# Kernel optimization log

Measured on AMD Instinct MI355X. Metric: run time of the kernel, lower is better.

The kernel has to match this reference:

```python
import jax, jax.numpy as jnp
import numpy as np

B, S, MD, H = 8, 1024, 1024, 16
D = MD // H  # 64
# Faithful to torch: scale = (dim_per_head // num_heads) ** -0.5 (a quirk, not 1/sqrt(D))
SCALE = float((D // H) ** (-0.5))


def setup_inputs() -> dict:
    k0 = jax.random.key(0)
    ks = jax.random.split(k0, 11)
    w = 1.0 / np.sqrt(MD)
    mk = lambda k, shape, s: jax.random.normal(k, shape, dtype=jnp.float32) * s
    return {
        "query": mk(ks[0], (B, S, MD), 1.0),
        "key": mk(ks[1], (B, S, MD), 1.0),
        "value": mk(ks[2], (B, S, MD), 1.0),
        "Wq": mk(ks[3], (MD, MD), w), "bq": mk(ks[4], (MD,), w),
        "Wk": mk(ks[5], (MD, MD), w), "bk": mk(ks[6], (MD,), w),
        "Wv": mk(ks[7], (MD, MD), w), "bv": mk(ks[8], (MD,), w),
        "Wo": mk(ks[9], (MD, MD), w), "bo": mk(ks[10], (MD,), w),
    }


def reference(query, key, value, Wq, bq, Wk, bk, Wv, bv, Wo, bo):
    # Dropout is identity in eval mode (deterministic reference).
    Bq, T, _ = query.shape
    Sk = key.shape[1]
    q = query @ Wq + bq   # [B, T, H*D]
    k = key @ Wk + bk     # [B, S, H*D]
    v = value @ Wv + bv
    # Faithful replication of torch .view(B*H, -1, D): plain row-major reshape
    # (NOT a head transpose -- it chunks sequence/head indices together).
    q = q.reshape(Bq * H, T, D)
    k = k.reshape(Bq * H, Sk, D)
    v = v.reshape(Bq * H, Sk, D)
    attn = jnp.einsum('btd,bsd->bts', q, k) * SCALE          # [B*H, T, S]
    p = jax.nn.softmax(attn, axis=-1)
    ctx = jnp.einsum('bts,bsd->btd', p, v).reshape(Bq, T, H * D)
    output = ctx @ Wo + bo                                    # [B, T, MD]
    a = attn.reshape(Bq, H, T, Sk)
    attn_post = jax.nn.sigmoid(a).sum(axis=1) / H             # [B, T, S]
    return output, attn_post
```

## Files before the change

kernel.cpp:

```cpp
#include <hip/hip_runtime.h>


typedef __attribute__((ext_vector_type(8))) short bf16x8;
typedef __attribute__((ext_vector_type(4))) float f32x4;
typedef __attribute__((ext_vector_type(4))) int int4v;

static __device__ __forceinline__ short f2bf(float f) {
  union { float f; unsigned u; } v; v.f = f;
  unsigned lsb = (v.u >> 16) & 1u;
  v.u += 0x7fffu + lsb;
  return (short)(v.u >> 16);
}

#define GLDS16(gp, lp) __builtin_amdgcn_global_load_lds( \
    (const __attribute__((address_space(1))) void*)(gp), \
    (__attribute__((address_space(3))) void*)(lp), 16, 0, 0)

__global__ __launch_bounds__(256) void convt_f32(
    const float* __restrict__ src, short* __restrict__ dst)
{
  __shared__ float T[64][65];
  const int tid = threadIdx.x;
  const int c0 = blockIdx.x * 64, r0 = blockIdx.y * 64;
  {
    const int rr = tid >> 4, cc = (tid & 15) * 4;
    for (int i = 0; i < 4; ++i) {
      int row = rr + i * 16;
      const float4 v = *(const float4*)(src + (size_t)(r0 + row) * 1024 + c0 + cc);
      T[row][cc] = v.x; T[row][cc + 1] = v.y; T[row][cc + 2] = v.z; T[row][cc + 3] = v.w;
    }
  }
  __syncthreads();
  {
    const int rr = tid >> 3, cc = (tid & 7) * 8;
    for (int i = 0; i < 2; ++i) {
      int row = rr + i * 32;
      bf16x8 v;
      for (int j = 0; j < 8; ++j) v[j] = f2bf(T[cc + j][row]);
      *(bf16x8*)(dst + (size_t)(c0 + row) * 1024 + r0 + cc) = v;
    }
  }
}

__global__ __launch_bounds__(256) void cvt_bf16(
    const float* __restrict__ src, short* __restrict__ dst)
{
  const size_t i = ((size_t)blockIdx.x * 256 + threadIdx.x) * 8;
  const float4 v0 = *(const float4*)(src + i);
  const float4 v1 = *(const float4*)(src + i + 4);
  bf16x8 o;
  o[0] = f2bf(v0.x); o[1] = f2bf(v0.y); o[2] = f2bf(v0.z); o[3] = f2bf(v0.w);
  o[4] = f2bf(v1.x); o[5] = f2bf(v1.y); o[6] = f2bf(v1.z); o[7] = f2bf(v1.w);
  *(bf16x8*)(dst + i) = o;
}

__global__ __launch_bounds__(256) void transp_v(
    const short* __restrict__ src, short* __restrict__ dst)
{
  __shared__ short T[64][72];
  const int g = blockIdx.y, t0 = blockIdx.x * 64;
  const short* s = src + (size_t)g * 65536 + (size_t)t0 * 64;
  short* d = dst + (size_t)g * 65536 + t0;
  const int r = threadIdx.x >> 3, c = (threadIdx.x & 7) * 8;
  for (int i = 0; i < 2; ++i) {
    bf16x8 v = *(const bf16x8*)(s + (size_t)(r + i * 32) * 64 + c);
    *(bf16x8*)(&T[r + i * 32][c]) = v;
  }
  __syncthreads();
  for (int i = 0; i < 2; ++i) {
    int dr = r + i * 32;
    bf16x8 v;
    for (int j = 0; j < 8; ++j) v[j] = T[c + j][dr];
    *(bf16x8*)(d + (size_t)dr * 1024 + c) = v;
  }
}

__global__ __launch_bounds__(256) void gemm_bt16(
    const short* __restrict__ A, const short* __restrict__ BT,
    const float* __restrict__ bias, void* __restrict__ Cp,
    int mode, int M, int N, int K)
{
  __shared__ short As[128 * 64];
  __shared__ short Bs[128 * 64];
  const int tid = threadIdx.x;
  const int lane = tid & 63, wave = tid >> 6;
  const int quad = lane >> 4, l16 = lane & 15;
  const int wm = (wave & 1) * 64, wn = (wave >> 1) * 64;
  const int bm = blockIdx.x * 128, bn = blockIdx.y * 128;

  f32x4 acc[4][4] = {};

  const int s_row = tid >> 3;
  const int s_col = (tid & 7) * 8;
  const int lds_base = wave * 512;

  for (int k0 = 0; k0 < K; k0 += 64) {
    for (int i = 0; i < 4; ++i) {
      int row = s_row + i * 32;
      GLDS16(A + (size_t)(bm + row) * K + k0 + s_col, &As[i * 2048 + lds_base]);
      GLDS16(BT + (size_t)(bn + row) * K + k0 + s_col, &Bs[i * 2048 + lds_base]);
    }
    __syncthreads();
    for (int ks = 0; ks < 2; ++ks) {
      bf16x8 af[4], bfr[4];
      for (int mi = 0; mi < 4; ++mi)
        af[mi] = *(const bf16x8*)(&As[(wm + mi * 16 + l16) * 64 + ks * 32 + quad * 8]);
      for (int ni = 0; ni < 4; ++ni)
        bfr[ni] = *(const bf16x8*)(&Bs[(wn + ni * 16 + l16) * 64 + ks * 32 + quad * 8]);
      for (int mi = 0; mi < 4; ++mi)
        for (int ni = 0; ni < 4; ++ni)
          acc[mi][ni] = __builtin_amdgcn_mfma_f32_16x16x32_bf16(af[mi], bfr[ni], acc[mi][ni], 0, 0, 0);
    }
    __syncthreads();
  }

  for (int ni = 0; ni < 4; ++ni) {
    int col = bn + wn + ni * 16 + l16;
    float bv = bias[col];
    for (int mi = 0; mi < 4; ++mi) {
      int row0 = bm + wm + mi * 16 + quad * 4;
      for (int r = 0; r < 4; ++r) {
        int row = row0 + r;
        float fv = acc[mi][ni][r] + bv;
        if (mode == 2) ((float*)Cp)[(size_t)row * N + col] = fv;
        else           ((short*)Cp)[(size_t)row * N + col] = f2bf(fv);
      }
    }
  }
}

__global__ __launch_bounds__(256) void attn_fused(
    const short* __restrict__ Qp, const short* __restrict__ Kp,
    const short* __restrict__ VpT,
    short* __restrict__ ctx,
    float* __restrict__ attn_post)
{
  __shared__ short Plds[16][1032];
  __shared__ float red[16][4];
  __shared__ float ctxred[4][16][64];

  const int tid = threadIdx.x;
  const int wave = tid >> 6, lane = tid & 63;
  const int quad = lane >> 4, l16 = lane & 15;
  const int b = blockIdx.x >> 6;
  const int t0 = (blockIdx.x & 63) * 16;
  const int sbase = wave * 256;

  float sig[16][4] = {};

  for (int h = 0; h < 16; ++h) {
    const int g = b * 16 + h;
    const short* Qg = Qp + (size_t)g * 65536;
    const short* Kg = Kp + (size_t)g * 65536;
    const short* Vg = VpT + (size_t)g * 65536;

    bf16x8 aq0 = *(const bf16x8*)(Qg + (t0 + l16) * 64 + quad * 8);
    bf16x8 aq1 = *(const bf16x8*)(Qg + (t0 + l16) * 64 + 32 + quad * 8);

    float sc[16][4];
    float rsum[4] = {0.f, 0.f, 0.f, 0.f};
    for (int tile = 0; tile < 16; ++tile) {
      int s = sbase + tile * 16;
      bf16x8 bk0 = *(const bf16x8*)(Kg + (s + l16) * 64 + quad * 8);
      bf16x8 bk1 = *(const bf16x8*)(Kg + (s + l16) * 64 + 32 + quad * 8);
      f32x4 c = {0.f, 0.f, 0.f, 0.f};
      c = __builtin_amdgcn_mfma_f32_16x16x32_bf16(aq0, bk0, c, 0, 0, 0);
      c = __builtin_amdgcn_mfma_f32_16x16x32_bf16(aq1, bk1, c, 0, 0, 0);
      for (int r = 0; r < 4; ++r) {
        float x = c[r] * 0.5f;
        float e = __expf(x);
        sc[tile][r] = e;
        rsum[r] += e;
        sig[tile][r] += e * __builtin_amdgcn_rcpf(1.f + e);
      }
    }
    for (int r = 0; r < 4; ++r)
      for (int mask = 1; mask < 16; mask <<= 1) rsum[r] += __shfl_xor(rsum[r], mask, 64);
    if (l16 == 0)
      for (int r = 0; r < 4; ++r) red[quad * 4 + r][wave] = rsum[r];
    __syncthreads();
    for (int r = 0; r < 4; ++r) {
      int row = quad * 4 + r;
      float s4 = red[row][0] + red[row][1] + red[row][2] + red[row][3];
      float inv = __builtin_amdgcn_rcpf(s4);
      for (int tile = 0; tile < 16; ++tile)
        Plds[row][sbase + tile * 16 + l16] = f2bf(sc[tile][r] * inv);
    }
    f32x4 cacc[4] = {};
    for (int ks = 0; ks < 8; ++ks) {
      bf16x8 ap = *(const bf16x8*)(&Plds[l16][sbase + ks * 32 + quad * 8]);
      for (int ni = 0; ni < 4; ++ni) {
        bf16x8 bv = *(const bf16x8*)(Vg + (ni * 16 + l16) * 1024 + sbase + ks * 32 + quad * 8);
        cacc[ni] = __builtin_amdgcn_mfma_f32_16x16x32_bf16(ap, bv, cacc[ni], 0, 0, 0);
      }
    }
    for (int ni = 0; ni < 4; ++ni)
      for (int r = 0; r < 4; ++r)
        ctxred[wave][quad * 4 + r][ni * 16 + l16] = cacc[ni][r];
    __syncthreads();
    short* ctxg = ctx + (size_t)g * 65536 + t0 * 64;
    for (int e = tid; e < 1024; e += 256) {
      int t = e >> 6, dd = e & 63;
      float v = ctxred[0][t][dd] + ctxred[1][t][dd] + ctxred[2][t][dd] + ctxred[3][t][dd];
      ctxg[t * 64 + dd] = f2bf(v);
    }
  }

  float* ap_out = attn_post + (size_t)b * 1048576 + (size_t)t0 * 1024;
  for (int tile = 0; tile < 16; ++tile)
    for (int r = 0; r < 4; ++r)
      ap_out[(quad * 4 + r) * 1024 + sbase + tile * 16 + l16] = sig[tile][r] * 0.0625f;
}

extern "C" void kernel_launch(void* const* d_in, const int* in_sizes, int n_in,
                              void* d_out, int out_size, void* d_ws, size_t ws_size,
                              hipStream_t stream) {
  const float* query = (const float*)d_in[0];
  const float* key   = (const float*)d_in[1];
  const float* value = (const float*)d_in[2];
  const float* Wq = (const float*)d_in[3]; const float* bq = (const float*)d_in[4];
  const float* Wk = (const float*)d_in[5]; const float* bk = (const float*)d_in[6];
  const float* Wv = (const float*)d_in[7]; const float* bv = (const float*)d_in[8];
  const float* Wo = (const float*)d_in[9]; const float* bo = (const float*)d_in[10];

  short* WqT   = (short*)d_ws;
  short* WkT   = WqT + (1u << 20);
  short* WvT   = WkT + (1u << 20);
  short* WoT   = WvT + (1u << 20);
  short* Qp    = WoT + (1u << 20);
  short* Kp    = Qp + (8u << 20);
  short* VpT   = Kp + (8u << 20);
  short* Xin   = VpT + (8u << 20);
  short* Vflat = Xin + (8u << 20);
  short* ctx   = Xin;

  float* out0 = (float*)d_out;
  float* attn_post = out0 + (8u << 20);

  dim3 blk(256);
  dim3 ggrid(64, 8);
  convt_f32<<<dim3(16, 16), blk, 0, stream>>>(Wq, WqT);
  convt_f32<<<dim3(16, 16), blk, 0, stream>>>(Wk, WkT);
  convt_f32<<<dim3(16, 16), blk, 0, stream>>>(Wv, WvT);
  convt_f32<<<dim3(16, 16), blk, 0, stream>>>(Wo, WoT);

  cvt_bf16<<<dim3(4096), blk, 0, stream>>>(query, Xin);
  gemm_bt16<<<ggrid, blk, 0, stream>>>(Xin, WqT, bq, Qp, 0, 8192, 1024, 1024);
  cvt_bf16<<<dim3(4096), blk, 0, stream>>>(key, Xin);
  gemm_bt16<<<ggrid, blk, 0, stream>>>(Xin, WkT, bk, Kp, 0, 8192, 1024, 1024);
  cvt_bf16<<<dim3(4096), blk, 0, stream>>>(value, Xin);
  gemm_bt16<<<ggrid, blk, 0, stream>>>(Xin, WvT, bv, Vflat, 0, 8192, 1024, 1024);
  transp_v<<<dim3(16, 128), blk, 0, stream>>>(Vflat, VpT);

  attn_fused<<<dim3(512), blk, 0, stream>>>(Qp, Kp, VpT, ctx, attn_post);
  gemm_bt16<<<ggrid, blk, 0, stream>>>(ctx, WoT, bo, out0, 2, 8192, 1024, 1024);
}
```

Measured before the change: 553.8 us.

## Batch QKV projections, split attention heads across blocks with atomic sigmoid accumulation

Merges the four weight transposes and the three input conversions and QKV GEMMs into single z-indexed launches when the workspace is large enough, cutting launch count and letting the three GEMMs run concurrently. The attention kernel now splits the 16 heads into two groups per block, doubling the grid to 1024 blocks for better occupancy. Because each block now holds only half the heads, the sigmoid-mean output must be combined with float atomicAdd into a buffer zeroed by an extra kernel. Per-wave P staging is reused for the context reduction, which shrinks LDS use. The costs are the extra zeroing pass, atomic traffic on a 32 MB output, and non-deterministic summation order.

```diff
diff --git a/kernel.cpp b/kernel.cpp
--- a/kernel.cpp
+++ b/kernel.cpp
@@ -16,9 +16,14 @@
     (const __attribute__((address_space(1))) void*)(gp), \
     (__attribute__((address_space(3))) void*)(lp), 16, 0, 0)
 
-__global__ __launch_bounds__(256) void convt_f32(
-    const float* __restrict__ src, short* __restrict__ dst)
-{
+struct Ptr4 { const float* s[4]; short* d[4]; };
+struct Ptr3 { const float* s[3]; short* d[3]; };
+struct QkvArgs { const short* A[3]; const short* B[3]; const float* bias[3]; short* C[3]; };
+
+__global__ __launch_bounds__(256) void convt4(Ptr4 a)
+{
+  const float* __restrict__ src = a.s[blockIdx.z];
+  short* __restrict__ dst = a.d[blockIdx.z];
   __shared__ float T[64][65];
   const int tid = threadIdx.x;
   const int c0 = blockIdx.x * 64, r0 = blockIdx.y * 64;
@@ -42,9 +47,10 @@
   }
 }
 
-__global__ __launch_bounds__(256) void cvt_bf16(
-    const float* __restrict__ src, short* __restrict__ dst)
-{
+__global__ __launch_bounds__(256) void cvt3(Ptr3 a)
+{
+  const float* __restrict__ src = a.s[blockIdx.z];
+  short* __restrict__ dst = a.d[blockIdx.z];
   const size_t i = ((size_t)blockIdx.x * 256 + threadIdx.x) * 8;
   const float4 v0 = *(const float4*)(src + i);
   const float4 v1 = *(const float4*)(src + i + 4);
@@ -52,6 +58,14 @@
   o[0] = f2bf(v0.x); o[1] = f2bf(v0.y); o[2] = f2bf(v0.z); o[3] = f2bf(v0.w);
   o[4] = f2bf(v1.x); o[5] = f2bf(v1.y); o[6] = f2bf(v1.z); o[7] = f2bf(v1.w);
   *(bf16x8*)(dst + i) = o;
+}
+
+__global__ __launch_bounds__(256) void zero_f32(float* __restrict__ p)
+{
+  const size_t i = ((size_t)blockIdx.x * 256 + threadIdx.x) * 16;
+  const float4 z = {0.f, 0.f, 0.f, 0.f};
+  *(float4*)(p + i) = z; *(float4*)(p + i + 4) = z;
+  *(float4*)(p + i + 8) = z; *(float4*)(p + i + 12) = z;
 }
 
 __global__ __launch_bounds__(256) void transp_v(
@@ -75,13 +89,13 @@
   }
 }
 
-__global__ __launch_bounds__(256) void gemm_bt16(
+static __device__ __forceinline__ void gemm_body(
     const short* __restrict__ A, const short* __restrict__ BT,
-    const float* __restrict__ bias, void* __restrict__ Cp,
-    int mode, int M, int N, int K)
+    const float* __restrict__ bias, void* __restrict__ Cp, int mode)
 {
   __shared__ short As[128 * 64];
   __shared__ short Bs[128 * 64];
+  const int K = 1024, N = 1024;
   const int tid = threadIdx.x;
   const int lane = tid & 63, wave = tid >> 6;
   const int quad = lane >> 4, l16 = lane & 15;
@@ -129,26 +143,39 @@
   }
 }
 
-__global__ __launch_bounds__(256) void attn_fused(
+__global__ __launch_bounds__(256) void gemm_bt16(
+    const short* __restrict__ A, const short* __restrict__ BT,
+    const float* __restrict__ bias, void* __restrict__ Cp, int mode)
+{
+  gemm_body(A, BT, bias, Cp, mode);
+}
+
+__global__ __launch_bounds__(256) void gemm_qkv(QkvArgs a)
+{
+  const int z = blockIdx.z;
+  gemm_body(a.A[z], a.B[z], a.bias[z], a.C[z], 0);
+}
+
+__global__ __launch_bounds__(256) void attn_fused2(
     const short* __restrict__ Qp, const short* __restrict__ Kp,
     const short* __restrict__ VpT,
     short* __restrict__ ctx,
     float* __restrict__ attn_post)
 {
-  __shared__ short Plds[16][1032];
+  __shared__ short Pw[4][16][264];
   __shared__ float red[16][4];
-  __shared__ float ctxred[4][16][64];
 
   const int tid = threadIdx.x;
   const int wave = tid >> 6, lane = tid & 63;
   const int quad = lane >> 4, l16 = lane & 15;
-  const int b = blockIdx.x >> 6;
-  const int t0 = (blockIdx.x & 63) * 16;
+  const int hg = blockIdx.x & 1;
+  const int t0 = ((blockIdx.x >> 1) & 63) * 16;
+  const int b = blockIdx.x >> 7;
   const int sbase = wave * 256;
 
   float sig[16][4] = {};
 
-  for (int h = 0; h < 16; ++h) {
+  for (int h = hg * 8; h < hg * 8 + 8; ++h) {
     const int g = b * 16 + h;
     const short* Qg = Qp + (size_t)g * 65536;
     const short* Kg = Kp + (size_t)g * 65536;
@@ -184,24 +211,30 @@
       float s4 = red[row][0] + red[row][1] + red[row][2] + red[row][3];
       float inv = __builtin_amdgcn_rcpf(s4);
       for (int tile = 0; tile < 16; ++tile)
-        Plds[row][sbase + tile * 16 + l16] = f2bf(sc[tile][r] * inv);
+        Pw[wave][row][tile * 16 + l16] = f2bf(sc[tile][r] * inv);
     }
     f32x4 cacc[4] = {};
     for (int ks = 0; ks < 8; ++ks) {
-      bf16x8 ap = *(const bf16x8*)(&Plds[l16][sbase + ks * 32 + quad * 8]);
+      bf16x8 ap = *(const bf16x8*)(&Pw[wave][l16][ks * 32 + quad * 8]);
       for (int ni = 0; ni < 4; ++ni) {
         bf16x8 bv = *(const bf16x8*)(Vg + (ni * 16 + l16) * 1024 + sbase + ks * 32 + quad * 8);
         cacc[ni] = __builtin_amdgcn_mfma_f32_16x16x32_bf16(ap, bv, cacc[ni], 0, 0, 0);
       }
     }
-    for (int ni = 0; ni < 4; ++ni)
-      for (int r = 0; r < 4; ++r)
-        ctxred[wave][quad * 4 + r][ni * 16 + l16] = cacc[ni][r];
+    {
+      float* cw = (float*)(&Pw[wave][0][0]);
+      for (int ni = 0; ni < 4; ++ni)
+        for (int r = 0; r < 4; ++r)
+          cw[(quad * 4 + r) * 64 + ni * 16 + l16] = cacc[ni][r];
+    }
     __syncthreads();
     short* ctxg = ctx + (size_t)g * 65536 + t0 * 64;
     for (int e = tid; e < 1024; e += 256) {
       int t = e >> 6, dd = e & 63;
-      float v = ctxred[0][t][dd] + ctxred[1][t][dd] + ctxred[2][t][dd] + ctxred[3][t][dd];
+      float v = ((float*)(&Pw[0][0][0]))[t * 64 + dd]
+              + ((float*)(&Pw[1][0][0]))[t * 64 + dd]
+              + ((float*)(&Pw[2][0][0]))[t * 64 + dd]
+              + ((float*)(&Pw[3][0][0]))[t * 64 + dd];
       ctxg[t * 64 + dd] = f2bf(v);
     }
   }
@@ -209,7 +242,8 @@
   float* ap_out = attn_post + (size_t)b * 1048576 + (size_t)t0 * 1024;
   for (int tile = 0; tile < 16; ++tile)
     for (int r = 0; r < 4; ++r)
-      ap_out[(quad * 4 + r) * 1024 + sbase + tile * 16 + l16] = sig[tile][r] * 0.0625f;
+      atomicAdd(&ap_out[(quad * 4 + r) * 1024 + sbase + tile * 16 + l16],
+                sig[tile][r] * 0.0625f);
 }
 
 extern "C" void kernel_launch(void* const* d_in, const int* in_sizes, int n_in,
@@ -223,35 +257,50 @@
   const float* Wv = (const float*)d_in[7]; const float* bv = (const float*)d_in[8];
   const float* Wo = (const float*)d_in[9]; const float* bo = (const float*)d_in[10];
 
-  short* WqT   = (short*)d_ws;
-  short* WkT   = WqT + (1u << 20);
-  short* WvT   = WkT + (1u << 20);
-  short* WoT   = WvT + (1u << 20);
-  short* Qp    = WoT + (1u << 20);
-  short* Kp    = Qp + (8u << 20);
-  short* VpT   = Kp + (8u << 20);
-  short* Xin   = VpT + (8u << 20);
-  short* Vflat = Xin + (8u << 20);
-  short* ctx   = Xin;
-
   float* out0 = (float*)d_out;
   float* attn_post = out0 + (8u << 20);
 
+  short* WqT = (short*)d_ws;
+  short* WkT = WqT + (1u << 20);
+  short* WvT = WkT + (1u << 20);
+  short* WoT = WvT + (1u << 20);
+  short* Qp  = WoT + (1u << 20);
+  short* Kp  = Qp + (8u << 20);
+  short* VpT = Kp + (8u << 20);
+
   dim3 blk(256);
-  dim3 ggrid(64, 8);
-  convt_f32<<<dim3(16, 16), blk, 0, stream>>>(Wq, WqT);
-  convt_f32<<<dim3(16, 16), blk, 0, stream>>>(Wk, WkT);
-  convt_f32<<<dim3(16, 16), blk, 0, stream>>>(Wv, WvT);
-  convt_f32<<<dim3(16, 16), blk, 0, stream>>>(Wo, WoT);
-
-  cvt_bf16<<<dim3(4096), blk, 0, stream>>>(query, Xin);
-  gemm_bt16<<<ggrid, blk, 0, stream>>>(Xin, WqT, bq, Qp, 0, 8192, 1024, 1024);
-  cvt_bf16<<<dim3(4096), blk, 0, stream>>>(key, Xin);
-  gemm_bt16<<<ggrid, blk, 0, stream>>>(Xin, WkT, bk, Kp, 0, 8192, 1024, 1024);
-  cvt_bf16<<<dim3(4096), blk, 0, stream>>>(value, Xin);
-  gemm_bt16<<<ggrid, blk, 0, stream>>>(Xin, WvT, bv, Vflat, 0, 8192, 1024, 1024);
-  transp_v<<<dim3(16, 128), blk, 0, stream>>>(Vflat, VpT);
-
-  attn_fused<<<dim3(512), blk, 0, stream>>>(Qp, Kp, VpT, ctx, attn_post);
-  gemm_bt16<<<ggrid, blk, 0, stream>>>(ctx, WoT, bo, out0, 2, 8192, 1024, 1024);
-}
+  const size_t NEED_BIG = (size_t)(60u << 20) * 2;
+
+  convt4<<<dim3(16, 16, 4), blk, 0, stream>>>(
+      Ptr4{{Wq, Wk, Wv, Wo}, {WqT, WkT, WvT, WoT}});
+  zero_f32<<<dim3(2048), blk, 0, stream>>>(attn_post);
+
+  short* ctx;
+  if (ws_size >= NEED_BIG) {
+    short* Xq = VpT + (8u << 20);
+    short* Xk = Xq + (8u << 20);
+    short* Xv = Xk + (8u << 20);
+    short* Vflat = Xv + (8u << 20);
+    ctx = Xq;
+
+    cvt3<<<dim3(4096, 1, 3), blk, 0, stream>>>(Ptr3{{query, key, value}, {Xq, Xk, Xv}});
+    gemm_qkv<<<dim3(64, 8, 3), blk, 0, stream>>>(
+        QkvArgs{{Xq, Xk, Xv}, {WqT, WkT, WvT}, {bq, bk, bv}, {Qp, Kp, Vflat}});
+    transp_v<<<dim3(16, 128), blk, 0, stream>>>(Vflat, VpT);
+  } else {
+    short* Xin = VpT + (8u << 20);
+    short* Vflat = Xin + (8u << 20);
+    ctx = Xin;
+
+    cvt3<<<dim3(4096, 1, 1), blk, 0, stream>>>(Ptr3{{query, query, query}, {Xin, Xin, Xin}});
+    gemm_bt16<<<dim3(64, 8), blk, 0, stream>>>(Xin, WqT, bq, Qp, 0);
+    cvt3<<<dim3(4096, 1, 1), blk, 0, stream>>>(Ptr3{{key, key, key}, {Xin, Xin, Xin}});
+    gemm_bt16<<<dim3(64, 8), blk, 0, stream>>>(Xin, WkT, bk, Kp, 0);
+    cvt3<<<dim3(4096, 1, 1), blk, 0, stream>>>(Ptr3{{value, value, value}, {Xin, Xin, Xin}});
+    gemm_bt16<<<dim3(64, 8), blk, 0, stream>>>(Xin, WvT, bv, Vflat, 0);
+    transp_v<<<dim3(16, 128), blk, 0, stream>>>(Vflat, VpT);
+  }
+
+  attn_fused2<<<dim3(1024), blk, 0, stream>>>(Qp, Kp, VpT, ctx, attn_post);
+  gemm_bt16<<<dim3(64, 8), blk, 0, stream>>>(ctx, WoT, bo, out0, 2);
+}
```

After: 566.2 us. 2.2% more time.
